# Kernel optimization log

Hardware: AMD Instinct MI355X
Metric: run time of the kernel (lower is better)

## Reference

```python
import jax, jax.numpy as jnp
import numpy as np

VOCAB, TAGS, EMB, HID = 50000, 32, 256, 512
H = HID // 2  # per-direction LSTM hidden size
B, T = 64, 512


def setup_inputs() -> dict:
    key = jax.random.key(0)
    ks = jax.random.split(key, 14)
    s = 0.05
    X = jax.random.randint(ks[0], (B, T), 0, VOCAB, dtype=jnp.int32)
    y = jax.random.randint(ks[1], (B, T), 0, TAGS, dtype=jnp.int32)
    embed = jax.random.normal(ks[2], (VOCAB, EMB), jnp.float32) * s
    # PyTorch LSTM layout: W_ih [4H, E], W_hh [4H, H], gate order i,f,g,o
    Wi_f = jax.random.normal(ks[3], (4 * H, EMB), jnp.float32) * s
    Wh_f = jax.random.normal(ks[4], (4 * H, H), jnp.float32) * s
    b_f = jnp.zeros((4 * H,), jnp.float32)
    Wi_b = jax.random.normal(ks[5], (4 * H, EMB), jnp.float32) * s
    Wh_b = jax.random.normal(ks[6], (4 * H, H), jnp.float32) * s
    b_b = jnp.zeros((4 * H,), jnp.float32)
    fcW = jax.random.normal(ks[7], (TAGS, HID), jnp.float32) * s
    fcb = jnp.zeros((TAGS,), jnp.float32)
    trans = jax.random.normal(ks[8], (TAGS, TAGS), jnp.float32) * s
    start = jax.random.normal(ks[9], (TAGS,), jnp.float32) * s
    end = jax.random.normal(ks[10], (TAGS,), jnp.float32) * s
    return {"X": X, "y": y, "embed": embed,
            "Wi_f": Wi_f, "Wh_f": Wh_f, "b_f": b_f,
            "Wi_b": Wi_b, "Wh_b": Wh_b, "b_b": b_b,
            "fcW": fcW, "fcb": fcb,
            "trans": trans, "start": start, "end": end}


def _lstm_dir(x, Wi, Wh, b, reverse):
    # x: [B, T, E] -> hs: [B, T, H]
    Bn = x.shape[0]
    WiT, WhT = Wi.T, Wh.T

    def step(carry, xt):
        h, c = carry
        g = xt @ WiT + h @ WhT + b  # [B, 4H]
        i, f, gg, o = jnp.split(g, 4, axis=-1)
        i, f, o = jax.nn.sigmoid(i), jax.nn.sigmoid(f), jax.nn.sigmoid(o)
        c = f * c + i * jnp.tanh(gg)
        h = o * jnp.tanh(c)
        return (h, c), h

    h0 = jnp.zeros((Bn, H), x.dtype)
    _, hs = jax.lax.scan(step, (h0, h0), jnp.swapaxes(x, 0, 1), reverse=reverse)
    return jnp.swapaxes(hs, 0, 1)


def _emissions(X, embed, Wi_f, Wh_f, b_f, Wi_b, Wh_b, b_b, fcW, fcb):
    x = embed[X]  # [B, T, E]
    hf = _lstm_dir(x, Wi_f, Wh_f, b_f, reverse=False)
    hb = _lstm_dir(x, Wi_b, Wh_b, b_b, reverse=True)
    h = jnp.concatenate([hf, hb], axis=-1)  # [B, T, HID]
    return h @ fcW.T + fcb  # [B, T, K]


def _crf_loss(em, y, trans, start, end):
    # log-partition via forward algorithm (full mask)
    alpha0 = start + em[:, 0]  # [B, K]

    def step(alpha, et):
        a = jax.nn.logsumexp(alpha[:, :, None] + trans[None], axis=1) + et
        return a, None

    alpha, _ = jax.lax.scan(step, alpha0, jnp.swapaxes(em[:, 1:], 0, 1))
    logZ = jax.nn.logsumexp(alpha + end, axis=-1)  # [B]
    # gold path score
    em_sc = jnp.take_along_axis(em, y[..., None].astype(jnp.int32), axis=-1)[..., 0].sum(-1)
    tr_sc = trans[y[:, :-1], y[:, 1:]].sum(-1)
    num = start[y[:, 0]] + em_sc + tr_sc + end[y[:, -1]]
    return -(num - logZ).mean()


def reference(X, y, embed, Wi_f, Wh_f, b_f, Wi_b, Wh_b, b_b, fcW, fcb, trans, start, end):
    em = _emissions(X, embed, Wi_f, Wh_f, b_f, Wi_b, Wh_b, b_b, fcW, fcb)
    return _crf_loss(em, y, trans, start, end)
```

## Files before the change

### kernel.cpp

```cpp
#include <hip/hip_runtime.h>
#include <hip/hip_fp16.h>
#include <stdint.h>

#define TAGS  32
#define EMB   256
#define HID   512
#define HSZ   256
#define G4H   1024
#define BATCH 64
#define TLEN  512

typedef _Float16 half8  __attribute__((ext_vector_type(8)));
typedef _Float16 half2v __attribute__((ext_vector_type(2)));
typedef float    f32x4  __attribute__((ext_vector_type(4)));
typedef int      i32x4  __attribute__((ext_vector_type(4)));
typedef unsigned int u32x4v __attribute__((ext_vector_type(4)));

#if defined(__has_builtin)
#if __has_builtin(__builtin_amdgcn_fdot2)
#define HAVE_FDOT2 1
#endif
#endif

__device__ __forceinline__ float fdot2f(unsigned a, unsigned b, float c) {
    half2v ha = __builtin_bit_cast(half2v, a);
    half2v hb = __builtin_bit_cast(half2v, b);
#ifdef HAVE_FDOT2
    return __builtin_amdgcn_fdot2(ha, hb, c, false);
#else
    return c + (float)ha[0]*(float)hb[0] + (float)ha[1]*(float)hb[1];
#endif
}
__device__ __forceinline__ float sigmoid_f(float x){ return 1.0f/(1.0f+__expf(-x)); }
__device__ __forceinline__ float tanh_f(float x){ return 1.0f - 2.0f/(__expf(2.0f*x)+1.0f); }

__device__ __forceinline__ void ldsbar() {
    asm volatile("s_waitcnt lgkmcnt(0)" ::: "memory");
    __builtin_amdgcn_sched_barrier(0);
    __builtin_amdgcn_s_barrier();
    __builtin_amdgcn_sched_barrier(0);
}

__global__ __launch_bounds__(256)
void whimg_kernel(const float* __restrict__ WhF, const float* __restrict__ WhB,
                  u32x4v* __restrict__ WhI8) {
    const int id = blockIdx.x * 256 + threadIdx.x;
    const int dir = id >> 14, r = id & 16383;
    const int lane = r & 63;
    const int ks = (r >> 6) & 3;
    const int gg = (r >> 8) & 7;
    const int w  = (r >> 11) & 7;
    const int n = (gg >> 1) * 256 + w * 32 + (gg & 1) * 16 + (lane & 15);
    const int k = ks * 64 + (lane >> 4) * 16;
    const float* src = (dir ? WhB : WhF) + (size_t)n * HSZ + k;
    u32x4v out;
#pragma unroll
    for (int d = 0; d < 4; ++d) {
        unsigned dw = 0;
#pragma unroll
        for (int e = 0; e < 4; ++e) {
            int q = __float2int_rn(src[d * 4 + e] * 256.0f);
            q = q > 127 ? 127 : (q < -127 ? -127 : q);
            dw |= ((unsigned)(q & 0xff)) << (8 * e);
        }
        out[d] = dw;
    }
    WhI8[id] = out;
}

__global__ __launch_bounds__(256)
void wiimg_kernel(const float* __restrict__ WiF, const float* __restrict__ WiB,
                  half8* __restrict__ WiT) {
    const int slot = blockIdx.x * 256 + threadIdx.x;
    const int lane = slot & 63;
    const int ks = (slot >> 6) & 7;
    const int nt = (slot >> 9) & 63;
    const int dir = slot >> 15;
    const int n = nt * 16 + (lane & 15);
    const int k = ks * 32 + (lane >> 4) * 8;
    const float* src = (dir ? WiB : WiF) + (size_t)n * EMB + k;
    half8 hv;
#pragma unroll
    for (int e = 0; e < 8; ++e) hv[e] = (_Float16)src[e];
    WiT[slot] = hv;
}

__global__ __launch_bounds__(512, 2)
void gemm_xwt_kernel(const int* __restrict__ X, const float* __restrict__ embed,
                     const half8* __restrict__ WiT, const float* __restrict__ bF,
                     const float* __restrict__ bB, __half* __restrict__ xWT) {
    const int t   = blockIdx.x;
    const int dir = blockIdx.y;
    const int tid = threadIdx.x;
    const int lane = tid & 63;
    const int w    = tid >> 6;
    const int mt   = w & 3;
    const int nh   = w >> 2;
    const int l15  = lane & 15;
    const int lp   = lane >> 4;
    const float* bias = dir ? bB : bF;

    __shared__ ushort A[4 * 8 * 64 * 8];

    {
        const int b = tid >> 3, ks = tid & 7;
        const int erow = X[b * TLEN + t];
        const float* src = embed + (size_t)erow * EMB + ks * 32;
        const int amt = b >> 4, bl = b & 15;
#pragma unroll
        for (int lpp = 0; lpp < 4; ++lpp) {
            const float4 x0 = *(const float4*)(src + lpp * 8);
            const float4 x1 = *(const float4*)(src + lpp * 8 + 4);
            half8 hv;
            hv[0]=(_Float16)x0.x; hv[1]=(_Float16)x0.y; hv[2]=(_Float16)x0.z; hv[3]=(_Float16)x0.w;
            hv[4]=(_Float16)x1.x; hv[5]=(_Float16)x1.y; hv[6]=(_Float16)x1.z; hv[7]=(_Float16)x1.w;
            *(half8*)&A[(((amt * 8 + ks) * 64) + lpp * 16 + bl) * 8] = hv;
        }
    }
    __syncthreads();

    half8 afr[8];
#pragma unroll
    for (int ks = 0; ks < 8; ++ks)
        afr[ks] = *(const half8*)&A[(((mt * 8 + ks) * 64) + lane) * 8];

    const half8* Bw = WiT + (size_t)(dir * 64 + nh * 32) * 8 * 64;

    half8 bcur[8], bnxt[8];
#pragma unroll
    for (int ks = 0; ks < 8; ++ks) bcur[ks] = Bw[(size_t)ks * 64 + lane];

#pragma unroll 4
    for (int j = 0; j < 32; ++j) {
        if (j < 31) {
#pragma unroll
            for (int ks = 0; ks < 8; ++ks)
                bnxt[ks] = Bw[((size_t)(j + 1) * 8 + ks) * 64 + lane];
        }
        f32x4 acc4 = {};
#pragma unroll
        for (int ks = 0; ks < 8; ++ks)
            acc4 = __builtin_amdgcn_mfma_f32_16x16x32_f16(afr[ks], bcur[ks], acc4, 0, 0, 0);

        const int nt = nh * 32 + j;
        const float bs = bias[nt * 16 + l15];
#pragma unroll
        for (int rr = 0; rr < 4; ++rr) {
            const int b = mt * 16 + lp * 4 + rr;
            const __half hh = __float2half(acc4[rr] + bs);
            xWT[((size_t)((dir * BATCH + b) * TLEN + t)) * G4H + nt * 16 + l15] = hh;
        }
#pragma unroll
        for (int ks = 0; ks < 8; ++ks) bcur[ks] = bnxt[ks];
    }
}


#define WBF1(SLOT, A0, A1, A2, A3)                                           \
    {                                                                        \
        const u32x4v v_ = base[(SLOT) * 64 + lane];                          \
        asm volatile("v_accvgpr_write_b32 a" A0 ", %0\n\t"                   \
                     "v_accvgpr_write_b32 a" A1 ", %1\n\t"                   \
                     "v_accvgpr_write_b32 a" A2 ", %2\n\t"                   \
                     "v_accvgpr_write_b32 a" A3 ", %3"                       \
                     :: "v"(v_[0]), "v"(v_[1]), "v"(v_[2]), "v"(v_[3])       \
                     : "a" A0, "a" A1, "a" A2, "a" A3);                      \
    }

#define MFMA1(ACC, S0, S3)                                                   \
    asm("v_mfma_i32_16x16x64_i8 %0, %1, a[" S0 ":" S3 "], %0"                \
        : "+v"(ACC) : "v"(areg))

__global__ __launch_bounds__(512, 2)
void lstm_kernel(const __half* __restrict__ xWT,
                 const u32x4v* __restrict__ WhI8,
                 __half* __restrict__ hist) {
    const int bg  = blockIdx.x;
    const int dir = blockIdx.y;
    const int tid = threadIdx.x;
    const int lane = tid & 63;
    const int w    = tid >> 6;
    const int l15  = lane & 15;
    const int lp   = lane >> 4;

    __shared__ signed char h8[2 * 256];
    __shared__ int gbuf[4 * 256];

    const __half* xwD = xWT + (size_t)(dir * BATCH + bg) * ((size_t)TLEN * G4H);
    __half* hD = hist + (size_t)(dir * BATCH + bg) * TLEN * HSZ;

    {
        const u32x4v* base = WhI8 + (size_t)(dir * 8 + w) * 2048;
        WBF1( 0,  "0",  "1",  "2",  "3")  WBF1( 1,  "4",  "5",  "6",  "7")
        WBF1( 2,  "8",  "9", "10", "11")  WBF1( 3, "12", "13", "14", "15")
        WBF1( 4, "16", "17", "18", "19")  WBF1( 5, "20", "21", "22", "23")
        WBF1( 6, "24", "25", "26", "27")  WBF1( 7, "28", "29", "30", "31")
        WBF1( 8, "32", "33", "34", "35")  WBF1( 9, "36", "37", "38", "39")
        WBF1(10, "40", "41", "42", "43")  WBF1(11, "44", "45", "46", "47")
        WBF1(12, "48", "49", "50", "51")  WBF1(13, "52", "53", "54", "55")
        WBF1(14, "56", "57", "58", "59")  WBF1(15, "60", "61", "62", "63")
        WBF1(16, "64", "65", "66", "67")  WBF1(17, "68", "69", "70", "71")
        WBF1(18, "72", "73", "74", "75")  WBF1(19, "76", "77", "78", "79")
        WBF1(20, "80", "81", "82", "83")  WBF1(21, "84", "85", "86", "87")
        WBF1(22, "88", "89", "90", "91")  WBF1(23, "92", "93", "94", "95")
        WBF1(24, "96", "97", "98", "99")  WBF1(25, "100", "101", "102", "103")
        WBF1(26, "104", "105", "106", "107") WBF1(27, "108", "109", "110", "111")
        WBF1(28, "112", "113", "114", "115") WBF1(29, "116", "117", "118", "119")
        WBF1(30, "120", "121", "122", "123") WBF1(31, "124", "125", "126", "127")
        asm volatile("s_nop 7\n\ts_nop 7" :::);
    }

    for (int i = tid; i < 128; i += 512) ((unsigned int*)h8)[i] = 0;

    float c0 = 0.0f;
    ushort xwc[4], xwn[4];
    if (tid < 256) {
        const __half* p0 = xwD + (size_t)(dir ? (TLEN - 1) : 0) * G4H;
#pragma unroll
        for (int g = 0; g < 4; ++g)
            xwc[g] = __half_as_ushort(p0[g * 256 + tid]);
    }
    __syncthreads();

    i32x4 acc[8];
    int p = 0;
    for (int ts = 0; ts < TLEN; ++ts) {
        const int t = dir ? (TLEN - 1 - ts) : ts;
        const signed char* h8r = h8 + p * 256;

#pragma unroll
        for (int gg = 0; gg < 8; ++gg) { i32x4 z = {0,0,0,0}; acc[gg] = z; }

#define KS_BLOCK(KS, P0a,P0b, P1a,P1b, P2a,P2b, P3a,P3b, P4a,P4b, P5a,P5b, P6a,P6b, P7a,P7b) \
        {                                                                                    \
            const u32x4v areg = *(const u32x4v*)(h8r + (KS) * 64 + lp * 16);                 \
            MFMA1(acc[0], P0a, P0b); MFMA1(acc[1], P1a, P1b);                                \
            MFMA1(acc[2], P2a, P2b); MFMA1(acc[3], P3a, P3b);                                \
            MFMA1(acc[4], P4a, P4b); MFMA1(acc[5], P5a, P5b);                                \
            MFMA1(acc[6], P6a, P6b); MFMA1(acc[7], P7a, P7b);                                \
        }
        KS_BLOCK(0,  "0","3",  "16","19", "32","35", "48","51", "64","67", "80","83", "96","99",  "112","115")
        KS_BLOCK(1,  "4","7",  "20","23", "36","39", "52","55", "68","71", "84","87", "100","103","116","119")
        KS_BLOCK(2,  "8","11", "24","27", "40","43", "56","59", "72","75", "88","91", "104","107","120","123")
        KS_BLOCK(3, "12","15", "28","31", "44","47", "60","63", "76","79", "92","95", "108","111","124","127")
#undef KS_BLOCK

        if (lane < 16) {
            const int ubase = w * 32 + l15;
#pragma unroll
            for (int gg = 0; gg < 8; ++gg)
                gbuf[(gg >> 1) * 256 + ubase + (gg & 1) * 16] = acc[gg][0];
        }
        ldsbar();

        if (tid < 256) {
            const int u = tid;
            const float inv = 3.0757688e-5f;
            const float gi = (float)__ushort_as_half(xwc[0]) + (float)gbuf[0 * 256 + u] * inv;
            const float gf = (float)__ushort_as_half(xwc[1]) + (float)gbuf[1 * 256 + u] * inv;
            const float gz = (float)__ushort_as_half(xwc[2]) + (float)gbuf[2 * 256 + u] * inv;
            const float go = (float)__ushort_as_half(xwc[3]) + (float)gbuf[3 * 256 + u] * inv;
            const float ig = sigmoid_f(gi);
            const float fg = sigmoid_f(gf);
            const float gv = tanh_f(gz);
            const float og = sigmoid_f(go);
            c0 = fg * c0 + ig * gv;
            const float hv = og * tanh_f(c0);
            hD[(size_t)t * HSZ + u] = __float2half(hv);
            h8[(p ^ 1) * 256 + u] = (signed char)__float2int_rn(hv * 127.0f);
            const int tn = dir ? (t > 0 ? t - 1 : 0) : (t < TLEN - 1 ? t + 1 : t);
            const __half* pp = xwD + (size_t)tn * G4H;
#pragma unroll
            for (int g = 0; g < 4; ++g)
                xwn[g] = __half_as_ushort(pp[g * 256 + u]);
        }
        ldsbar();

        if (tid < 256) {
#pragma unroll
            for (int g = 0; g < 4; ++g) xwc[g] = xwn[g];
        }
        p ^= 1;
    }
}
#undef WBF1
#undef MFMA1

__global__ __launch_bounds__(256)
void em_kernel(const __half* __restrict__ hist, const float* __restrict__ fcW,
               float* __restrict__ em) {
    const int b   = blockIdx.x >> 3;
    const int t0  = (blockIdx.x & 7) * 64;
    const int tid = threadIdx.x;

    __shared__ ushort hf[64][264];
    __shared__ ushort hb[64][264];
    __shared__ ushort fcs[32][520];

    for (int i = tid; i < 32 * 128; i += 256) {
        const int k = i >> 7, j4 = i & 127;
        const float4 f = *(const float4*)&fcW[(size_t)k * HID + j4 * 4];
        unsigned long long pk =
              (unsigned long long)__half_as_ushort(__float2half(f.x))
            | ((unsigned long long)__half_as_ushort(__float2half(f.y)) << 16)
            | ((unsigned long long)__half_as_ushort(__float2half(f.z)) << 32)
            | ((unsigned long long)__half_as_ushort(__float2half(f.w)) << 48);
        *(unsigned long long*)&fcs[k][j4 * 4] = pk;
    }
    const __half* hfp = hist;
    const __half* hbp = hist + (size_t)BATCH * TLEN * HSZ;
    for (int i = tid; i < 64 * 32; i += 256) {
        const int row = i >> 5, seg = i & 31;
        const uint4 vf = *(const uint4*)(hfp + ((size_t)b * TLEN + t0 + row) * HSZ + seg*8);
        const uint4 vb = *(const uint4*)(hbp + ((size_t)b * TLEN + t0 + row) * HSZ + seg*8);
        *(uint4*)&hf[row][seg*8] = vf;
        *(uint4*)&hb[row][seg*8] = vb;
    }
    __syncthreads();

    const int tok = tid >> 2;
    const int kq  = tid & 3;
    float s[8] = {0,0,0,0,0,0,0,0};
    for (int j2 = 0; j2 < 128; ++j2) {
        const unsigned hfv = *(const unsigned*)&hf[tok][j2*2];
        const unsigned hbv = *(const unsigned*)&hb[tok][j2*2];
#pragma unroll
        for (int kk = 0; kk < 8; ++kk) {
            const int k = kq*8 + kk;
            s[kk] = fdot2f(hfv, *(const unsigned*)&fcs[k][j2*2], s[kk]);
            s[kk] = fdot2f(hbv, *(const unsigned*)&fcs[k][256 + j2*2], s[kk]);
        }
    }
    float* dst = em + ((size_t)b * TLEN + t0 + tok) * TAGS + kq*8;
#pragma unroll
    for (int kk = 0; kk < 8; ++kk) dst[kk] = s[kk];
}

__global__ __launch_bounds__(128)
void crf_kernel(const float* __restrict__ em, const float* __restrict__ fcb,
                const float* __restrict__ trans, const float* __restrict__ startv,
                const float* __restrict__ endv, const int* __restrict__ y,
                float* __restrict__ partial) {
    const int b   = blockIdx.x;
    const int tid = threadIdx.x;
    const int tag = tid >> 2, q = tid & 3;

    __shared__ float alpha[2][TAGS];
    __shared__ float trs[TAGS][TAGS + 1];
    __shared__ float gpart[2];
    __shared__ float logZs;

    for (int i = tid; i < TAGS * TAGS; i += 128)
        trs[i >> 5][i & 31] = trans[i];

    const float* e = em + (size_t)b * TLEN * TAGS;

    if (tid < TAGS)
        alpha[0][tid] = startv[tid] + e[tid] + fcb[tid];
    __syncthreads();

    const float fcbt = fcb[tag];
    float ecur = e[TAGS + tag];
    int p = 0;
    for (int t = 1; t < TLEN; ++t) {
        float vs[8], m = -3.0e38f;
#pragma unroll
        for (int i = 0; i < 8; ++i) {
            const float v = alpha[p][q * 8 + i] + trs[q * 8 + i][tag];
            vs[i] = v; m = fmaxf(m, v);
        }
        m = fmaxf(m, __shfl_xor(m, 1, 64));
        m = fmaxf(m, __shfl_xor(m, 2, 64));
        float s = 0.0f;
#pragma unroll
        for (int i = 0; i < 8; ++i) s += __expf(vs[i] - m);
        s += __shfl_xor(s, 1, 64);
        s += __shfl_xor(s, 2, 64);
        const int tn = (t + 1 < TLEN) ? (t + 1) : t;
        const float enext = e[(size_t)tn * TAGS + tag];
        if (q == 0) alpha[p ^ 1][tag] = m + __logf(s) + ecur + fcbt;
        __syncthreads();
        ecur = enext;
        p ^= 1;
    }

    {
        const float v = (tid < TAGS) ? (alpha[p][tid] + endv[tid]) : -3.0e38f;
        if (tid < 64) {
            float mx = v;
#pragma unroll
            for (int off = 32; off; off >>= 1) mx = fmaxf(mx, __shfl_xor(mx, off, 64));
            float ex = (tid < TAGS) ? __expf(v - mx) : 0.0f;
#pragma unroll
            for (int off = 32; off; off >>= 1) ex += __shfl_xor(ex, off, 64);
            if (tid == 0) logZs = mx + __logf(ex);
        }
    }

    const int* yb = y + (size_t)b * TLEN;
    float gsum = 0.0f;
    for (int t = tid; t < TLEN; t += 128) {
        const int yt = yb[t];
        gsum += e[t * TAGS + yt] + fcb[yt];
    }
    for (int t = tid; t < TLEN - 1; t += 128)
        gsum += trans[yb[t] * TAGS + yb[t + 1]];
#pragma unroll
    for (int off = 32; off; off >>= 1) gsum += __shfl_xor(gsum, off, 64);
    if ((tid & 63) == 0) gpart[tid >> 6] = gsum;
    __syncthreads();
    if (tid == 0) {
        const float num = startv[yb[0]] + gpart[0] + gpart[1] + endv[yb[TLEN - 1]];
        partial[b] = logZs - num;
    }
}

__global__ void reduce_kernel(const float* __restrict__ partial, float* __restrict__ out) {
    float v = partial[threadIdx.x];
#pragma unroll
    for (int off = 32; off; off >>= 1) v += __shfl_xor(v, off, 64);
    if (threadIdx.x == 0) out[0] = v * (1.0f / BATCH);
}

extern "C" void kernel_launch(void* const* d_in, const int* in_sizes, int n_in,
                              void* d_out, int out_size, void* d_ws, size_t ws_size,
                              hipStream_t stream) {
    (void)in_sizes; (void)n_in; (void)out_size; (void)ws_size;

    const int*   X      = (const int*)  d_in[0];
    const int*   y      = (const int*)  d_in[1];
    const float* embed  = (const float*)d_in[2];
    const float* Wi_f   = (const float*)d_in[3];
    const float* Wh_f   = (const float*)d_in[4];
    const float* b_f    = (const float*)d_in[5];
    const float* Wi_b   = (const float*)d_in[6];
    const float* Wh_b   = (const float*)d_in[7];
    const float* b_b    = (const float*)d_in[8];
    const float* fcW    = (const float*)d_in[9];
    const float* fcb    = (const float*)d_in[10];
    const float* trans  = (const float*)d_in[11];
    const float* startv = (const float*)d_in[12];
    const float* endv   = (const float*)d_in[13];
    float* out = (float*)d_out;

    char* ws = (char*)d_ws;
    __half* xWT  = (__half*)(ws);
    float*  em   = (float*) (ws);
    __half* hist = (__half*)(ws + 134217728);
    u32x4v* WhI8 = (u32x4v*)(ws + 167772160);
    half8*  WiT  = (half8*) (ws + 168296448);
    float*  prt  = (float*) (ws + 169345024);

    whimg_kernel<<<128, 256, 0, stream>>>(Wh_f, Wh_b, WhI8);
    wiimg_kernel<<<256, 256, 0, stream>>>(Wi_f, Wi_b, WiT);

    dim3 ggrid(TLEN, 2);
    gemm_xwt_kernel<<<ggrid, 512, 0, stream>>>(X, embed, WiT, b_f, b_b, xWT);

    dim3 lgrid(BATCH, 2);
    lstm_kernel<<<lgrid, 512, 0, stream>>>(xWT, WhI8, hist);

    em_kernel<<<BATCH * 8, 256, 0, stream>>>(hist, fcW, em);

    crf_kernel<<<BATCH, 128, 0, stream>>>(em, fcb, trans, startv, endv, y, prt);

    reduce_kernel<<<1, 64, 0, stream>>>(prt, out);
}
```

Baseline: 957.0 us.

## Reuse B fragments across two M tiles in xW GEMM; single-wave CRF kernel

The input-projection GEMM now has each wave compute two 16-row batch tiles against the same weight fragments, over 16 column tiles instead of 32. This halves global weight-fragment loads per MFMA at the cost of more registers. The CRF forward recursion now runs as one 64-thread wavefront per batch item, with two lanes per tag. That replaces block-wide __syncthreads with a lighter LDS barrier (ldsbar) and removes cross-wave reductions through shared memory. In exchange, each lane does 16 logsumexp terms instead of 8.

After: 967.8 us. No clear change (+1.1%).

```diff
diff --git a/kernel.cpp b/kernel.cpp
--- a/kernel.cpp
+++ b/kernel.cpp
@@ -94,8 +94,8 @@
     const int tid = threadIdx.x;
     const int lane = tid & 63;
     const int w    = tid >> 6;
-    const int mt   = w & 3;
-    const int nh   = w >> 2;
+    const int mtp  = (w >> 2) * 2;
+    const int nq   = w & 3;
     const int l15  = lane & 15;
     const int lp   = lane >> 4;
     const float* bias = dir ? bB : bF;
@@ -119,36 +119,43 @@
     }
     __syncthreads();
 
-    half8 afr[8];
-#pragma unroll
-    for (int ks = 0; ks < 8; ++ks)
-        afr[ks] = *(const half8*)&A[(((mt * 8 + ks) * 64) + lane) * 8];
-
-    const half8* Bw = WiT + (size_t)(dir * 64 + nh * 32) * 8 * 64;
+    half8 afr[2][8];
+#pragma unroll
+    for (int e = 0; e < 2; ++e)
+#pragma unroll
+        for (int ks = 0; ks < 8; ++ks)
+            afr[e][ks] = *(const half8*)&A[((((mtp + e) * 8 + ks) * 64) + lane) * 8];
+
+    const half8* Bw = WiT + (size_t)(dir * 64 + nq * 16) * 8 * 64;
 
     half8 bcur[8], bnxt[8];
 #pragma unroll
     for (int ks = 0; ks < 8; ++ks) bcur[ks] = Bw[(size_t)ks * 64 + lane];
 
 #pragma unroll 4
-    for (int j = 0; j < 32; ++j) {
-        if (j < 31) {
+    for (int j = 0; j < 16; ++j) {
+        if (j < 15) {
 #pragma unroll
             for (int ks = 0; ks < 8; ++ks)
                 bnxt[ks] = Bw[((size_t)(j + 1) * 8 + ks) * 64 + lane];
         }
-        f32x4 acc4 = {};
-#pragma unroll
-        for (int ks = 0; ks < 8; ++ks)
-            acc4 = __builtin_amdgcn_mfma_f32_16x16x32_f16(afr[ks], bcur[ks], acc4, 0, 0, 0);
-
-        const int nt = nh * 32 + j;
+        f32x4 acc0 = {}, acc1 = {};
+#pragma unroll
+        for (int ks = 0; ks < 8; ++ks) {
+            acc0 = __builtin_amdgcn_mfma_f32_16x16x32_f16(afr[0][ks], bcur[ks], acc0, 0, 0, 0);
+            acc1 = __builtin_amdgcn_mfma_f32_16x16x32_f16(afr[1][ks], bcur[ks], acc1, 0, 0, 0);
+        }
+
+        const int nt = nq * 16 + j;
         const float bs = bias[nt * 16 + l15];
 #pragma unroll
         for (int rr = 0; rr < 4; ++rr) {
-            const int b = mt * 16 + lp * 4 + rr;
-            const __half hh = __float2half(acc4[rr] + bs);
-            xWT[((size_t)((dir * BATCH + b) * TLEN + t)) * G4H + nt * 16 + l15] = hh;
+            const int b0 = mtp * 16 + lp * 4 + rr;
+            const int b1 = b0 + 16;
+            xWT[((size_t)((dir * BATCH + b0) * TLEN + t)) * G4H + nt * 16 + l15] =
+                __float2half(acc0[rr] + bs);
+            xWT[((size_t)((dir * BATCH + b1) * TLEN + t)) * G4H + nt * 16 + l15] =
+                __float2half(acc1[rr] + bs);
         }
 #pragma unroll
         for (int ks = 0; ks < 8; ++ks) bcur[ks] = bnxt[ks];
@@ -336,82 +343,73 @@
     for (int kk = 0; kk < 8; ++kk) dst[kk] = s[kk];
 }
 
-__global__ __launch_bounds__(128)
+__global__ __launch_bounds__(64)
 void crf_kernel(const float* __restrict__ em, const float* __restrict__ fcb,
                 const float* __restrict__ trans, const float* __restrict__ startv,
                 const float* __restrict__ endv, const int* __restrict__ y,
                 float* __restrict__ partial) {
     const int b   = blockIdx.x;
     const int tid = threadIdx.x;
-    const int tag = tid >> 2, q = tid & 3;
+    const int tag = tid >> 1, q = tid & 1;
 
     __shared__ float alpha[2][TAGS];
     __shared__ float trs[TAGS][TAGS + 1];
-    __shared__ float gpart[2];
-    __shared__ float logZs;
-
-    for (int i = tid; i < TAGS * TAGS; i += 128)
+
+    for (int i = tid; i < TAGS * TAGS; i += 64)
         trs[i >> 5][i & 31] = trans[i];
 
     const float* e = em + (size_t)b * TLEN * TAGS;
 
     if (tid < TAGS)
         alpha[0][tid] = startv[tid] + e[tid] + fcb[tid];
-    __syncthreads();
+    ldsbar();
 
     const float fcbt = fcb[tag];
     float ecur = e[TAGS + tag];
     int p = 0;
     for (int t = 1; t < TLEN; ++t) {
-        float vs[8], m = -3.0e38f;
-#pragma unroll
-        for (int i = 0; i < 8; ++i) {
-            const float v = alpha[p][q * 8 + i] + trs[q * 8 + i][tag];
+        float vs[16], m = -3.0e38f;
+#pragma unroll
+        for (int i = 0; i < 16; ++i) {
+            const float v = alpha[p][q * 16 + i] + trs[q * 16 + i][tag];
             vs[i] = v; m = fmaxf(m, v);
         }
         m = fmaxf(m, __shfl_xor(m, 1, 64));
-        m = fmaxf(m, __shfl_xor(m, 2, 64));
         float s = 0.0f;
 #pragma unroll
-        for (int i = 0; i < 8; ++i) s += __expf(vs[i] - m);
+        for (int i = 0; i < 16; ++i) s += __expf(vs[i] - m);
         s += __shfl_xor(s, 1, 64);
-        s += __shfl_xor(s, 2, 64);
         const int tn = (t + 1 < TLEN) ? (t + 1) : t;
         const float enext = e[(size_t)tn * TAGS + tag];
         if (q == 0) alpha[p ^ 1][tag] = m + __logf(s) + ecur + fcbt;
-        __syncthreads();
+        ldsbar();
         ecur = enext;
         p ^= 1;
     }
 
-    {
-        const float v = (tid < TAGS) ? (alpha[p][tid] + endv[tid]) : -3.0e38f;
-        if (tid < 64) {
-            float mx = v;
-#pragma unroll
-            for (int off = 32; off; off >>= 1) mx = fmaxf(mx, __shfl_xor(mx, off, 64));
-            float ex = (tid < TAGS) ? __expf(v - mx) : 0.0f;
-#pragma unroll
-            for (int off = 32; off; off >>= 1) ex += __shfl_xor(ex, off, 64);
-            if (tid == 0) logZs = mx + __logf(ex);
-        }
-    }
+    const float v = (tid < TAGS) ? (alpha[p][tid] + endv[tid]) : -3.0e38f;
+    float mx = v;
+#pragma unroll
+    for (int off = 32; off; off >>= 1) mx = fmaxf(mx, __shfl_xor(mx, off, 64));
+    float ex = (tid < TAGS) ? __expf(v - mx) : 0.0f;
+#pragma unroll
+    for (int off = 32; off; off >>= 1) ex += __shfl_xor(ex, off, 64);
+    const float logZ = mx + __logf(ex);
 
     const int* yb = y + (size_t)b * TLEN;
     float gsum = 0.0f;
-    for (int t = tid; t < TLEN; t += 128) {
+    for (int t = tid; t < TLEN; t += 64) {
         const int yt = yb[t];
         gsum += e[t * TAGS + yt] + fcb[yt];
     }
-    for (int t = tid; t < TLEN - 1; t += 128)
+    for (int t = tid; t < TLEN - 1; t += 64)
         gsum += trans[yb[t] * TAGS + yb[t + 1]];
 #pragma unroll
     for (int off = 32; off; off >>= 1) gsum += __shfl_xor(gsum, off, 64);
-    if ((tid & 63) == 0) gpart[tid >> 6] = gsum;
-    __syncthreads();
+
     if (tid == 0) {
-        const float num = startv[yb[0]] + gpart[0] + gpart[1] + endv[yb[TLEN - 1]];
-        partial[b] = logZs - num;
+        const float num = startv[yb[0]] + gsum + endv[yb[TLEN - 1]];
+        partial[b] = logZ - num;
     }
 }
 
@@ -462,7 +460,7 @@
 
     em_kernel<<<BATCH * 8, 256, 0, stream>>>(hist, fcW, em);
 
-    crf_kernel<<<BATCH, 128, 0, stream>>>(em, fcb, trans, startv, endv, y, prt);
+    crf_kernel<<<BATCH, 64, 0, stream>>>(em, fcb, trans, startv, endv, y, prt);
 
     reduce_kernel<<<1, 64, 0, stream>>>(prt, out);
 }
```
